# Performance work log

Measured on AMD Instinct MI355X. Metric: run time of the kernel, lower is better.

Reference implementation:

```python
import jax, jax.numpy as jnp
import numpy as np

H = 12      # num attention heads
W = 128     # one-sided window size (band = 2W+1), also the chunk size
G = 32      # number of global tokens (positions 0..G-1)
NEG = -1e9


def setup_inputs() -> dict:
    key = jax.random.key(0)
    ks = jax.random.split(key, 9)
    B, S, D = 1, 4096, 768
    std = 0.02
    f32 = jnp.float32
    return {
        "hidden_states": jax.random.normal(ks[0], (B, S, D), f32),
        "Wq": jax.random.normal(ks[1], (D, D), f32) * std,
        "bq": jnp.zeros((D,), f32),
        "Wk": jax.random.normal(ks[2], (D, D), f32) * std,
        "bk": jnp.zeros((D,), f32),
        "Wv": jax.random.normal(ks[3], (D, D), f32) * std,
        "bv": jnp.zeros((D,), f32),
        "Wo": jax.random.normal(ks[4], (D, D), f32) * std,
        "bo": jnp.zeros((D,), f32),
    }


def _longformer_attn(hidden, Wq, bq, Wk, bk, Wv, bv, Wo, bo):
    B, S, D = hidden.shape
    dh = D // H
    scale = jnp.asarray(dh, hidden.dtype) ** -0.5

    def proj(Wm, bm):
        return (hidden @ Wm + bm).reshape(B, S, H, dh).transpose(0, 2, 1, 3)  # [B,H,S,dh]

    q = proj(Wq, bq) * scale
    k = proj(Wk, bk)
    v = proj(Wv, bv)

    nc = S // W  # number of query chunks
    q_ch = q.reshape(B, H, nc, W, dh)

    # pad keys/values by one chunk on each side; chunk c sees keys [c*W - W, c*W + 2W)
    kp = jnp.pad(k, ((0, 0), (0, 0), (W, W), (0, 0)))
    vp = jnp.pad(v, ((0, 0), (0, 0), (W, W), (0, 0)))
    idx = (jnp.arange(nc) * W)[:, None] + jnp.arange(3 * W)[None, :]  # [nc, 3W] into padded seq
    k_ch = kp[:, :, idx]  # [B,H,nc,3W,dh]
    v_ch = vp[:, :, idx]

    # banded scores via chunked matmul: [B,H,nc,W,3W]
    band = jnp.einsum('bhcqd,bhckd->bhcqk', q_ch, k_ch)

    # exact band mask |i-j| <= W: with local query qi and local key kj (global j = c*W + kj - W)
    qi = jnp.arange(W)[:, None]           # [W,1]
    kj = jnp.arange(3 * W)[None, :]       # [1,3W]
    in_band = (kj >= qi) & (kj <= qi + 2 * W)                     # [W,3W]
    j = (jnp.arange(nc) * W)[:, None, None] + kj[None] - W        # [nc,1,3W] global key index
    valid = in_band[None] & (j >= G) & (j < S)                    # [nc,W,3W]; j<G handled via global path
    band = jnp.where(valid[None, None], band, NEG)
    band = band.reshape(B, H, S, 3 * W)

    # every query also attends to the G global keys
    gsc = jnp.einsum('bhsd,bhgd->bhsg', q, k[:, :, :G])           # [B,H,S,G]
    scores = jnp.concatenate([gsc, band], axis=-1)                # [B,H,S,G+3W]
    probs = jax.nn.softmax(scores, axis=-1)

    out = jnp.einsum('bhsg,bhgd->bhsd', probs[..., :G], v[:, :, :G])
    pb = probs[..., G:].reshape(B, H, nc, W, 3 * W)
    out = out + jnp.einsum('bhcqk,bhckd->bhcqd', pb, v_ch).reshape(B, H, S, dh)

    # global queries attend to everything (full attention on G rows)
    gq_probs = jax.nn.softmax(jnp.einsum('bhgd,bhsd->bhgs', q[:, :, :G], k), axis=-1)
    out_g = jnp.einsum('bhgs,bhsd->bhgd', gq_probs, v)
    out = out.at[:, :, :G].set(out_g)

    out = out.transpose(0, 2, 1, 3).reshape(B, S, D)
    return out @ Wo + bo


def reference(hidden_states, Wq, bq, Wk, bk, Wv, bv, Wo, bo):
    return _longformer_attn(hidden_states, Wq, bq, Wk, bk, Wv, bv, Wo, bo)
```

## Files before the change

### kernel.cpp

```cpp
#include <hip/hip_runtime.h>
#include <stdint.h>

#define S_LEN 4096
#define DMOD  768
#define NH    12
#define DH    64
#define GG    32
#define NEGBIG (-1e9f)

typedef _Float16 f16;
typedef f16 f16x8 __attribute__((ext_vector_type(8)));
typedef f16 f16x4 __attribute__((ext_vector_type(4)));
typedef float f32x4 __attribute__((ext_vector_type(4)));
typedef uint32_t u32;

#define OFF_H16   ((size_t)0)
#define OFF_WT    ((size_t)6291456)
#define OFF_Q     ((size_t)11010048)
#define OFF_K     ((size_t)17301504)
#define OFF_V     ((size_t)23592960)
#define OFF_VT    ((size_t)29884416)
#define OFF_ATT   ((size_t)36175872)
#define OFF_GQO   ((size_t)42467328)
#define OFF_GQL   ((size_t)44040192)

__device__ __forceinline__ void gld_lds16(const void* g, void* l) {
  typedef __attribute__((address_space(3))) u32 lds_u32;
  typedef __attribute__((address_space(1))) u32 glb_u32;
  __builtin_amdgcn_global_load_lds((glb_u32*)(uintptr_t)g,
                                   (lds_u32*)(u32)(uintptr_t)l, 16, 0, 0);
}

__global__ __launch_bounds__(256) void prep_kernel(
    const float* __restrict__ hs,
    const float* __restrict__ Wq, const float* __restrict__ Wk,
    const float* __restrict__ Wv, const float* __restrict__ Wo,
    f16* __restrict__ h16, f16* __restrict__ wt)
{
  const int b = blockIdx.x;
  const int t = threadIdx.x;
  if (b < 576) {
    __shared__ float tile[64][65];
    const int w = b / 144, r2 = b % 144;
    const int n0 = (r2 % 12) * 64, k0 = (r2 / 12) * 64;
    const float* W = (w==0) ? Wq : (w==1) ? Wk : (w==2) ? Wv : Wo;
    f16* WT = wt + (size_t)w * DMOD * DMOD;
    #pragma unroll
    for (int rnd = 0; rnd < 4; ++rnd) {
      const int lin = rnd * 1024 + t * 4;
      const int r = lin >> 6, c = lin & 63;
      const float4 vv = *(const float4*)(W + (size_t)(k0 + r) * DMOD + n0 + c);
      tile[r][c+0] = vv.x; tile[r][c+1] = vv.y; tile[r][c+2] = vv.z; tile[r][c+3] = vv.w;
    }
    __syncthreads();
    #pragma unroll
    for (int rnd = 0; rnd < 2; ++rnd) {
      const int lin = rnd * 256 + t;
      const int n = lin >> 3, kc = (lin & 7) * 8;
      f16x8 o;
      #pragma unroll
      for (int j = 0; j < 8; ++j) o[j] = (f16)tile[kc + j][n];
      *(f16x8*)(WT + (size_t)(n0 + n) * DMOD + k0 + kc) = o;
    }
  } else {
    const size_t idx = (size_t)(b - 576) * 2048 + (size_t)t * 8;
    const float4 a = *(const float4*)(hs + idx);
    const float4 c = *(const float4*)(hs + idx + 4);
    f16x8 o;
    o[0]=(f16)a.x; o[1]=(f16)a.y; o[2]=(f16)a.z; o[3]=(f16)a.w;
    o[4]=(f16)c.x; o[5]=(f16)c.y; o[6]=(f16)c.z; o[7]=(f16)c.w;
    *(f16x8*)(h16 + idx) = o;
  }
}

__global__ __launch_bounds__(256) void gemm_qkv(
    const f16* __restrict__ A, const f16* __restrict__ wt,
    const float* __restrict__ bq, const float* __restrict__ bk, const float* __restrict__ bv,
    f16* __restrict__ q16, f16* __restrict__ k16, f16* __restrict__ v16)
{
  __shared__ __align__(16) f16 At[3][4096];
  __shared__ __align__(16) f16 Bt[3][4096];
  const int z = blockIdx.z;
  const f16* Wt = wt + (size_t)z * DMOD * DMOD;
  const float* bias = (z==0) ? bq : (z==1) ? bk : bv;
  f16* outp = (z==0) ? q16 : (z==1) ? k16 : v16;
  const float scale = (z==0) ? 0.125f : 1.0f;

  const int tid = threadIdx.x;
  const int lane = tid & 63, wid = tid >> 6;
  const int quad = lane >> 4, l15 = lane & 15;
  const int n0 = blockIdx.x * 128, m0 = blockIdx.y * 128;
  const int wm = (wid >> 1) * 64, wn = (wid & 1) * 64;

  f32x4 acc[4][4];
  #pragma unroll
  for (int i=0;i<4;++i)
    #pragma unroll
    for (int j=0;j<4;++j) acc[i][j] = (f32x4){0.f,0.f,0.f,0.f};

  const int lin0 = tid, lin1 = tid + 256;
  const int ar0 = ((lin0>>6)<<4) + (lin0&15), ac0 = ((lin0>>4)&3)*8;
  const int ar1 = ((lin1>>6)<<4) + (lin1&15), ac1 = ((lin1>>4)&3)*8;
  const f16* Ab = A  + (size_t)m0 * DMOD;
  const f16* Bb = Wt + (size_t)n0 * DMOD;

  gld_lds16(Ab + (size_t)ar0*DMOD + ac0, &At[0][lin0*8]);
  gld_lds16(Ab + (size_t)ar1*DMOD + ac1, &At[0][lin1*8]);
  gld_lds16(Bb + (size_t)ar0*DMOD + ac0, &Bt[0][lin0*8]);
  gld_lds16(Bb + (size_t)ar1*DMOD + ac1, &Bt[0][lin1*8]);

  int cur = 0;
  #pragma unroll 3
  for (int k = 0; k < 24; ++k) {
    const int nxt = (cur == 2) ? 0 : cur + 1;
    if (k < 23) {
      const int k0 = (k + 1) * 32;
      gld_lds16(Ab + (size_t)ar0*DMOD + k0 + ac0, &At[nxt][lin0*8]);
      gld_lds16(Ab + (size_t)ar1*DMOD + k0 + ac1, &At[nxt][lin1*8]);
      gld_lds16(Bb + (size_t)ar0*DMOD + k0 + ac0, &Bt[nxt][lin0*8]);
      gld_lds16(Bb + (size_t)ar1*DMOD + k0 + ac1, &Bt[nxt][lin1*8]);
      asm volatile("s_waitcnt vmcnt(4) lgkmcnt(0)" ::: "memory");
    } else {
      asm volatile("s_waitcnt vmcnt(0) lgkmcnt(0)" ::: "memory");
    }
    __builtin_amdgcn_s_barrier();
    f16x8 af[4], bf[4];
    #pragma unroll
    for (int i=0;i<4;++i) {
      af[i] = *(const f16x8*)(&At[cur][((wm>>4)+i)*512 + lane*8]);
      bf[i] = *(const f16x8*)(&Bt[cur][((wn>>4)+i)*512 + lane*8]);
    }
    #pragma unroll
    for (int i=0;i<4;++i)
      #pragma unroll
      for (int j=0;j<4;++j)
        acc[i][j] = __builtin_amdgcn_mfma_f32_16x16x32_f16(af[i], bf[j], acc[i][j], 0, 0, 0);
    cur = nxt;
  }

  #pragma unroll
  for (int j=0;j<4;++j) {
    const int col = n0 + wn + j*16 + l15;
    const float bcol = bias[col];
    const int h = col >> 6, d = col & 63;
    #pragma unroll
    for (int i=0;i<4;++i) {
      const int rbase = m0 + wm + i*16 + quad*4;
      f16* dst = outp + ((size_t)h * S_LEN + rbase) * DH + d;
      #pragma unroll
      for (int r=0;r<4;++r)
        dst[(size_t)r * DH] = (f16)((acc[i][j][r] + bcol) * scale);
    }
  }
}

__global__ __launch_bounds__(256) void gemm_out(
    const f16* __restrict__ A, const f16* __restrict__ Wt,
    const float* __restrict__ bo, float* __restrict__ outp)
{
  __shared__ __align__(16) f16 At[3][4096];
  __shared__ __align__(16) f16 Bt[3][2048];
  const int tid = threadIdx.x;
  const int lane = tid & 63, wid = tid >> 6;
  const int quad = lane >> 4, l15 = lane & 15;
  const int n0 = blockIdx.x * 64, m0 = blockIdx.y * 128;
  const int wm = (wid >> 1) * 64, wn = (wid & 1) * 32;

  f32x4 acc[4][2];
  #pragma unroll
  for (int i=0;i<4;++i)
    #pragma unroll
    for (int j=0;j<2;++j) acc[i][j] = (f32x4){0.f,0.f,0.f,0.f};

  const int lin0 = tid, lin1 = tid + 256;
  const int ar0 = ((lin0>>6)<<4) + (lin0&15), ac0 = ((lin0>>4)&3)*8;
  const int ar1 = ((lin1>>6)<<4) + (lin1&15), ac1 = ((lin1>>4)&3)*8;
  const f16* Ab = A  + (size_t)m0 * DMOD;
  const f16* Bb = Wt + (size_t)n0 * DMOD;

  gld_lds16(Ab + (size_t)ar0*DMOD + ac0, &At[0][lin0*8]);
  gld_lds16(Ab + (size_t)ar1*DMOD + ac1, &At[0][lin1*8]);
  gld_lds16(Bb + (size_t)ar0*DMOD + ac0, &Bt[0][lin0*8]);

  int cur = 0;
  #pragma unroll 3
  for (int k = 0; k < 24; ++k) {
    const int nxt = (cur == 2) ? 0 : cur + 1;
    if (k < 23) {
      const int k0 = (k + 1) * 32;
      gld_lds16(Ab + (size_t)ar0*DMOD + k0 + ac0, &At[nxt][lin0*8]);
      gld_lds16(Ab + (size_t)ar1*DMOD + k0 + ac1, &At[nxt][lin1*8]);
      gld_lds16(Bb + (size_t)ar0*DMOD + k0 + ac0, &Bt[nxt][lin0*8]);
      asm volatile("s_waitcnt vmcnt(3) lgkmcnt(0)" ::: "memory");
    } else {
      asm volatile("s_waitcnt vmcnt(0) lgkmcnt(0)" ::: "memory");
    }
    __builtin_amdgcn_s_barrier();
    f16x8 af[4], bf[2];
    #pragma unroll
    for (int i=0;i<4;++i)
      af[i] = *(const f16x8*)(&At[cur][((wm>>4)+i)*512 + lane*8]);
    #pragma unroll
    for (int j=0;j<2;++j)
      bf[j] = *(const f16x8*)(&Bt[cur][((wn>>4)+j)*512 + lane*8]);
    #pragma unroll
    for (int i=0;i<4;++i)
      #pragma unroll
      for (int j=0;j<2;++j)
        acc[i][j] = __builtin_amdgcn_mfma_f32_16x16x32_f16(af[i], bf[j], acc[i][j], 0, 0, 0);
    cur = nxt;
  }

  #pragma unroll
  for (int j=0;j<2;++j) {
    const int col = n0 + wn + j*16 + l15;
    const float bcol = bo[col];
    #pragma unroll
    for (int i=0;i<4;++i) {
      const int rbase = m0 + wm + i*16 + quad*4;
      #pragma unroll
      for (int r=0;r<4;++r)
        outp[(size_t)(rbase + r) * DMOD + col] = acc[i][j][r] + bcol;
    }
  }
}

__global__ __launch_bounds__(256) void v_transpose(const f16* __restrict__ v16,
                                                   f16* __restrict__ vt16)
{
  __shared__ f16 tile[64][72];
  const int st = blockIdx.x, h = blockIdx.y;
  const int t = threadIdx.x;
  const f16* src = v16 + (size_t)h * S_LEN * DH + (size_t)st * 64 * DH;
  #pragma unroll
  for (int rnd=0; rnd<2; ++rnd) {
    const int lin = rnd*256 + t;
    const int r = lin >> 3, c = (lin & 7) * 8;
    const f16x8 vv = *(const f16x8*)(src + (size_t)r * DH + c);
    #pragma unroll
    for (int j=0;j<8;++j) tile[r][c+j] = vv[j];
  }
  __syncthreads();
  f16* dst = vt16 + (size_t)h * DH * S_LEN + (size_t)st * 64;
  #pragma unroll
  for (int rnd=0; rnd<2; ++rnd) {
    const int lin = rnd*256 + t;
    const int d = lin >> 3, c = (lin & 7) * 8;
    f16x8 vv;
    #pragma unroll
    for (int j=0;j<8;++j) vv[j] = tile[c+j][d];
    *(f16x8*)(dst + (size_t)d * S_LEN + c) = vv;
  }
}

__global__ __launch_bounds__(256) void band_attn(
    const f16* __restrict__ q16, const f16* __restrict__ k16,
    const f16* __restrict__ vt16, f16* __restrict__ att16,
    float* __restrict__ o_part, float* __restrict__ l_part)
{
  __shared__ __align__(16) char smem[27648];
  __shared__ float lbuf[4][32];
  const int h = blockIdx.y;
  const int tid = threadIdx.x, lane = tid & 63, wid = tid >> 6;
  const int quad = lane >> 4, l15 = lane & 15;
  f16* P = (f16*)smem + wid * 1280;

  const f16* qh = q16 + (size_t)h * S_LEN * DH;
  const f16* kh = k16 + (size_t)h * S_LEN * DH;
  const f16* vh = vt16 + (size_t)h * DH * S_LEN;

  const bool is_gq = (blockIdx.x >= 127);
  const int gr0 = is_gq ? 0 : (blockIdx.x + 1) * 32;
  const int sp  = blockIdx.x - 127;

  f16x8 aq[2][2];
  #pragma unroll
  for (int mt=0;mt<2;++mt)
    #pragma unroll
    for (int ks=0;ks<2;++ks)
      aq[mt][ks] = *(const f16x8*)(qh + (size_t)(gr0 + mt*16 + l15)*DH + ks*32 + quad*8);

  f32x4 accO[2][4];
  float lacc[2][4];
  #pragma unroll
  for (int mt=0;mt<2;++mt) {
    #pragma unroll
    for (int n=0;n<4;++n) accO[mt][n] = (f32x4){0.f,0.f,0.f,0.f};
    #pragma unroll
    for (int r=0;r<4;++r) lacc[mt][r] = 0.f;
  }

  const int tstart = is_gq ? wid*2     : (wid==0) ? 0 : (wid==1) ? 2 : (wid==2) ? 5 : 8;
  const int tend   = is_gq ? wid*2 + 2 : (wid==0) ? 2 : (wid==1) ? 5 : (wid==2) ? 8 : 10;

  for (int t = tstart; t < tend; ++t) {
    int j0;
    if (is_gq) {
      j0 = sp*256 + t*32;
    } else if (t > 0) {
      j0 = gr0 - 128 + (t-1)*32;
      if (j0 <= 0 || j0 >= S_LEN) continue;
    } else {
      j0 = 0;
    }
    f16x8 bk[2][2];
    #pragma unroll
    for (int nt=0;nt<2;++nt) {
      const int key = j0 + nt*16 + l15;
      #pragma unroll
      for (int ks=0;ks<2;++ks)
        bk[nt][ks] = *(const f16x8*)(kh + (size_t)key*DH + ks*32 + quad*8);
    }
    f32x4 sc[2][2];
    #pragma unroll
    for (int mt=0;mt<2;++mt)
      #pragma unroll
      for (int nt=0;nt<2;++nt) {
        f32x4 s = __builtin_amdgcn_mfma_f32_16x16x32_f16(aq[mt][0], bk[nt][0],
                                                         (f32x4){0.f,0.f,0.f,0.f}, 0,0,0);
        sc[mt][nt] = __builtin_amdgcn_mfma_f32_16x16x32_f16(aq[mt][1], bk[nt][1], s, 0,0,0);
      }
    if (!is_gq && (t == 1 || t == 9)) {
      #pragma unroll
      for (int nt=0;nt<2;++nt)
        #pragma unroll
        for (int mt=0;mt<2;++mt)
          #pragma unroll
          for (int r=0;r<4;++r) {
            const int e = (nt*16 + l15) - (mt*16 + quad*4 + r);
            const bool ok = (t == 1) ? (e >= 0) : (e <= 0);
            if (!ok) sc[mt][nt][r] = NEGBIG;
          }
    }
    #pragma unroll
    for (int mt=0;mt<2;++mt)
      #pragma unroll
      for (int r=0;r<4;++r) {
        sc[mt][0][r] = __expf(sc[mt][0][r]);
        sc[mt][1][r] = __expf(sc[mt][1][r]);
        lacc[mt][r] += sc[mt][0][r] + sc[mt][1][r];
      }
    #pragma unroll
    for (int mt=0;mt<2;++mt)
      #pragma unroll
      for (int nt=0;nt<2;++nt)
        #pragma unroll
        for (int r=0;r<4;++r)
          P[(mt*16 + quad*4 + r)*40 + nt*16 + l15] = (f16)sc[mt][nt][r];
    asm volatile("s_waitcnt lgkmcnt(0)" ::: "memory");
    f16x8 ap[2];
    #pragma unroll
    for (int mt=0;mt<2;++mt)
      ap[mt] = *(const f16x8*)(P + (mt*16 + l15)*40 + quad*8);
    #pragma unroll
    for (int n=0;n<4;++n) {
      const f16x8 bv = *(const f16x8*)(vh + (size_t)(n*16 + l15)*S_LEN + j0 + quad*8);
      #pragma unroll
      for (int mt=0;mt<2;++mt)
        accO[mt][n] = __builtin_amdgcn_mfma_f32_16x16x32_f16(ap[mt], bv, accO[mt][n], 0,0,0);
    }
  }

  #pragma unroll
  for (int mt=0;mt<2;++mt)
    #pragma unroll
    for (int r=0;r<4;++r) {
      float v = lacc[mt][r];
      v += __shfl_xor(v, 1, 64);
      v += __shfl_xor(v, 2, 64);
      v += __shfl_xor(v, 4, 64);
      v += __shfl_xor(v, 8, 64);
      lacc[mt][r] = v;
    }

  __syncthreads();
  float* mbuf = (float*)smem;
  if (wid > 0) {
    #pragma unroll
    for (int mt=0;mt<2;++mt)
      #pragma unroll
      for (int n=0;n<4;++n)
        *(f32x4*)&mbuf[((wid-1)*64 + n*16 + l15)*36 + mt*16 + quad*4] = accO[mt][n];
  }
  if (l15 == 0) {
    #pragma unroll
    for (int mt=0;mt<2;++mt)
      #pragma unroll
      for (int r=0;r<4;++r)
        lbuf[wid][mt*16 + quad*4 + r] = lacc[mt][r];
  }
  __syncthreads();
  if (wid == 0) {
    #pragma unroll
    for (int w=0;w<3;++w)
      #pragma unroll
      for (int mt=0;mt<2;++mt)
        #pragma unroll
        for (int n=0;n<4;++n)
          accO[mt][n] += *(const f32x4*)&mbuf[(w*64 + n*16 + l15)*36 + mt*16 + quad*4];
    if (is_gq) {
      const int base = (h*16 + sp)*32;
      #pragma unroll
      for (int mt=0;mt<2;++mt)
        #pragma unroll
        for (int r=0;r<4;++r) {
          const int row = mt*16 + quad*4 + r;
          if (l15 == 0)
            l_part[base+row] = lbuf[0][row] + lbuf[1][row] + lbuf[2][row] + lbuf[3][row];
          #pragma unroll
          for (int n=0;n<4;++n)
            o_part[(size_t)(base+row)*DH + n*16 + l15] = accO[mt][n][r];
        }
    } else {
      #pragma unroll
      for (int mt=0;mt<2;++mt)
        #pragma unroll
        for (int r=0;r<4;++r) {
          const int row = mt*16 + quad*4 + r;
          const float lt = lbuf[0][row] + lbuf[1][row] + lbuf[2][row] + lbuf[3][row];
          const float inv = 1.f / lt;
          const int s = gr0 + row;
          #pragma unroll
          for (int n=0;n<4;++n)
            att16[(size_t)s * DMOD + h*DH + n*16 + l15] = (f16)(accO[mt][n][r] * inv);
        }
    }
  }
}

__global__ __launch_bounds__(256) void gq_merge(
    const float* __restrict__ o_part, const float* __restrict__ l_part,
    f16* __restrict__ att16)
{
  const int h = blockIdx.x;
  const int t = threadIdx.x;
  for (int u = t; u < 512; u += 256) {
    const int row = u >> 4, c4 = u & 15;
    float4 s = {0.f,0.f,0.f,0.f};
    float l = 0.f;
    for (int sp=0;sp<16;++sp) {
      const int base = (h*16 + sp)*32 + row;
      const float4 v = *(const float4*)&o_part[(size_t)base*DH + c4*4];
      s.x += v.x; s.y += v.y; s.z += v.z; s.w += v.w;
      l += l_part[base];
    }
    const float inv = 1.f / l;
    f16x4 o;
    o[0] = (f16)(s.x*inv); o[1] = (f16)(s.y*inv);
    o[2] = (f16)(s.z*inv); o[3] = (f16)(s.w*inv);
    *(f16x4*)&att16[(size_t)row * DMOD + h*DH + c4*4] = o;
  }
}

extern "C" void kernel_launch(void* const* d_in, const int* in_sizes, int n_in,
                              void* d_out, int out_size, void* d_ws, size_t ws_size,
                              hipStream_t stream)
{
  const float* hs = (const float*)d_in[0];
  const float* Wq = (const float*)d_in[1];
  const float* bq = (const float*)d_in[2];
  const float* Wk = (const float*)d_in[3];
  const float* bk = (const float*)d_in[4];
  const float* Wv = (const float*)d_in[5];
  const float* bv = (const float*)d_in[6];
  const float* Wo = (const float*)d_in[7];
  const float* bo = (const float*)d_in[8];
  float* out = (float*)d_out;
  char* ws = (char*)d_ws;
  f16* h16  = (f16*)(ws + OFF_H16);
  f16* wt   = (f16*)(ws + OFF_WT);
  f16* q16  = (f16*)(ws + OFF_Q);
  f16* k16  = (f16*)(ws + OFF_K);
  f16* v16  = (f16*)(ws + OFF_V);
  f16* vt16 = (f16*)(ws + OFF_VT);
  f16* att16= (f16*)(ws + OFF_ATT);
  float* gqo = (float*)(ws + OFF_GQO);
  float* gql = (float*)(ws + OFF_GQL);

  prep_kernel<<<2112, 256, 0, stream>>>(hs, Wq, Wk, Wv, Wo, h16, wt);
  gemm_qkv<<<dim3(6,32,3), 256, 0, stream>>>(h16, wt, bq, bk, bv, q16, k16, v16);
  v_transpose<<<dim3(64,12), 256, 0, stream>>>(v16, vt16);
  band_attn<<<dim3(143,12), 256, 0, stream>>>(q16, k16, vt16, att16, gqo, gql);
  gq_merge<<<12, 256, 0, stream>>>(gqo, gql, att16);
  gemm_out<<<dim3(12,32), 256, 0, stream>>>(att16, wt + (size_t)3*DMOD*DMOD, bo, out);
}
```

Baseline: 183.2 us.

## Fuse V transpose into QKV GEMM epilogue and give each wave independent band rows

The V projection epilogue now writes its output directly in transposed [h][d][s] layout, which removes the separate v_transpose kernel and its round trip through memory. band_attn is reorganised so each wave owns its own 32-row query group (or global-query split) for all key tiles, instead of four waves splitting the key tiles of one group. That drops the LDS cross-wave reduction and both barriers, and the grid shrinks from 143 to 36 blocks per head. The risks are strided 8-byte stores in the V epilogue and fewer blocks, which may lower occupancy and latency hiding.

```diff
diff --git a/kernel.cpp b/kernel.cpp
--- a/kernel.cpp
+++ b/kernel.cpp
@@ -18,7 +18,6 @@
 #define OFF_WT    ((size_t)6291456)
 #define OFF_Q     ((size_t)11010048)
 #define OFF_K     ((size_t)17301504)
-#define OFF_V     ((size_t)23592960)
 #define OFF_VT    ((size_t)29884416)
 #define OFF_ATT   ((size_t)36175872)
 #define OFF_GQO   ((size_t)42467328)
@@ -76,14 +75,13 @@
 __global__ __launch_bounds__(256) void gemm_qkv(
     const f16* __restrict__ A, const f16* __restrict__ wt,
     const float* __restrict__ bq, const float* __restrict__ bk, const float* __restrict__ bv,
-    f16* __restrict__ q16, f16* __restrict__ k16, f16* __restrict__ v16)
+    f16* __restrict__ q16, f16* __restrict__ k16, f16* __restrict__ vt16)
 {
   __shared__ __align__(16) f16 At[3][4096];
   __shared__ __align__(16) f16 Bt[3][4096];
   const int z = blockIdx.z;
   const f16* Wt = wt + (size_t)z * DMOD * DMOD;
   const float* bias = (z==0) ? bq : (z==1) ? bk : bv;
-  f16* outp = (z==0) ? q16 : (z==1) ? k16 : v16;
   const float scale = (z==0) ? 0.125f : 1.0f;
 
   const int tid = threadIdx.x;
@@ -138,18 +136,36 @@
     cur = nxt;
   }
 
-  #pragma unroll
-  for (int j=0;j<4;++j) {
-    const int col = n0 + wn + j*16 + l15;
-    const float bcol = bias[col];
-    const int h = col >> 6, d = col & 63;
-    #pragma unroll
-    for (int i=0;i<4;++i) {
-      const int rbase = m0 + wm + i*16 + quad*4;
-      f16* dst = outp + ((size_t)h * S_LEN + rbase) * DH + d;
-      #pragma unroll
-      for (int r=0;r<4;++r)
-        dst[(size_t)r * DH] = (f16)((acc[i][j][r] + bcol) * scale);
+  if (z < 2) {
+    f16* outp = (z==0) ? q16 : k16;
+    #pragma unroll
+    for (int j=0;j<4;++j) {
+      const int col = n0 + wn + j*16 + l15;
+      const float bcol = bias[col];
+      const int h = col >> 6, d = col & 63;
+      #pragma unroll
+      for (int i=0;i<4;++i) {
+        const int rbase = m0 + wm + i*16 + quad*4;
+        f16* dst = outp + ((size_t)h * S_LEN + rbase) * DH + d;
+        #pragma unroll
+        for (int r=0;r<4;++r)
+          dst[(size_t)r * DH] = (f16)((acc[i][j][r] + bcol) * scale);
+      }
+    }
+  } else {
+    #pragma unroll
+    for (int j=0;j<4;++j) {
+      const int col = n0 + wn + j*16 + l15;
+      const float bcol = bias[col];
+      const int h = col >> 6, d = col & 63;
+      #pragma unroll
+      for (int i=0;i<4;++i) {
+        const int rbase = m0 + wm + i*16 + quad*4;
+        f16x4 o;
+        #pragma unroll
+        for (int r=0;r<4;++r) o[r] = (f16)(acc[i][j][r] + bcol);
+        *(f16x4*)(vt16 + ((size_t)h * DH + d) * S_LEN + rbase) = o;
+      }
     }
   }
 }
@@ -225,54 +241,34 @@
   }
 }
 
-__global__ __launch_bounds__(256) void v_transpose(const f16* __restrict__ v16,
-                                                   f16* __restrict__ vt16)
-{
-  __shared__ f16 tile[64][72];
-  const int st = blockIdx.x, h = blockIdx.y;
-  const int t = threadIdx.x;
-  const f16* src = v16 + (size_t)h * S_LEN * DH + (size_t)st * 64 * DH;
-  #pragma unroll
-  for (int rnd=0; rnd<2; ++rnd) {
-    const int lin = rnd*256 + t;
-    const int r = lin >> 3, c = (lin & 7) * 8;
-    const f16x8 vv = *(const f16x8*)(src + (size_t)r * DH + c);
-    #pragma unroll
-    for (int j=0;j<8;++j) tile[r][c+j] = vv[j];
-  }
-  __syncthreads();
-  f16* dst = vt16 + (size_t)h * DH * S_LEN + (size_t)st * 64;
-  #pragma unroll
-  for (int rnd=0; rnd<2; ++rnd) {
-    const int lin = rnd*256 + t;
-    const int d = lin >> 3, c = (lin & 7) * 8;
-    f16x8 vv;
-    #pragma unroll
-    for (int j=0;j<8;++j) vv[j] = tile[c+j][d];
-    *(f16x8*)(dst + (size_t)d * S_LEN + c) = vv;
-  }
-}
-
 __global__ __launch_bounds__(256) void band_attn(
     const f16* __restrict__ q16, const f16* __restrict__ k16,
     const f16* __restrict__ vt16, f16* __restrict__ att16,
     float* __restrict__ o_part, float* __restrict__ l_part)
 {
-  __shared__ __align__(16) char smem[27648];
-  __shared__ float lbuf[4][32];
+  __shared__ __align__(16) f16 Pbuf[4][1280];
   const int h = blockIdx.y;
   const int tid = threadIdx.x, lane = tid & 63, wid = tid >> 6;
   const int quad = lane >> 4, l15 = lane & 15;
-  f16* P = (f16*)smem + wid * 1280;
+  f16* P = &Pbuf[wid][0];
+
+  const int bx = blockIdx.x;
+  const bool is_gq = (bx >= 32);
+  int gr0 = 0, sp = 0, tcount;
+  if (is_gq) {
+    sp = (bx - 32) * 4 + wid;
+    tcount = 8;
+  } else {
+    const int sub = bx * 4 + wid;
+    if (sub == 0) return;
+    gr0 = sub * 32;
+    tcount = 10;
+  }
 
   const f16* qh = q16 + (size_t)h * S_LEN * DH;
   const f16* kh = k16 + (size_t)h * S_LEN * DH;
   const f16* vh = vt16 + (size_t)h * DH * S_LEN;
 
-  const bool is_gq = (blockIdx.x >= 127);
-  const int gr0 = is_gq ? 0 : (blockIdx.x + 1) * 32;
-  const int sp  = blockIdx.x - 127;
-
   f16x8 aq[2][2];
   #pragma unroll
   for (int mt=0;mt<2;++mt)
@@ -290,10 +286,7 @@
     for (int r=0;r<4;++r) lacc[mt][r] = 0.f;
   }
 
-  const int tstart = is_gq ? wid*2     : (wid==0) ? 0 : (wid==1) ? 2 : (wid==2) ? 5 : 8;
-  const int tend   = is_gq ? wid*2 + 2 : (wid==0) ? 2 : (wid==1) ? 5 : (wid==2) ? 8 : 10;
-
-  for (int t = tstart; t < tend; ++t) {
+  for (int t = 0; t < tcount; ++t) {
     int j0;
     if (is_gq) {
       j0 = sp*256 + t*32;
@@ -373,58 +366,29 @@
       lacc[mt][r] = v;
     }
 
-  __syncthreads();
-  float* mbuf = (float*)smem;
-  if (wid > 0) {
-    #pragma unroll
-    for (int mt=0;mt<2;++mt)
-      #pragma unroll
-      for (int n=0;n<4;++n)
-        *(f32x4*)&mbuf[((wid-1)*64 + n*16 + l15)*36 + mt*16 + quad*4] = accO[mt][n];
-  }
-  if (l15 == 0) {
-    #pragma unroll
-    for (int mt=0;mt<2;++mt)
-      #pragma unroll
-      for (int r=0;r<4;++r)
-        lbuf[wid][mt*16 + quad*4 + r] = lacc[mt][r];
-  }
-  __syncthreads();
-  if (wid == 0) {
-    #pragma unroll
-    for (int w=0;w<3;++w)
-      #pragma unroll
-      for (int mt=0;mt<2;++mt)
+  if (is_gq) {
+    const int base = (h*16 + sp)*32;
+    #pragma unroll
+    for (int mt=0;mt<2;++mt)
+      #pragma unroll
+      for (int r=0;r<4;++r) {
+        const int row = mt*16 + quad*4 + r;
+        if (l15 == 0) l_part[base+row] = lacc[mt][r];
         #pragma unroll
         for (int n=0;n<4;++n)
-          accO[mt][n] += *(const f32x4*)&mbuf[(w*64 + n*16 + l15)*36 + mt*16 + quad*4];
-    if (is_gq) {
-      const int base = (h*16 + sp)*32;
-      #pragma unroll
-      for (int mt=0;mt<2;++mt)
-        #pragma unroll
-        for (int r=0;r<4;++r) {
-          const int row = mt*16 + quad*4 + r;
-          if (l15 == 0)
-            l_part[base+row] = lbuf[0][row] + lbuf[1][row] + lbuf[2][row] + lbuf[3][row];
-          #pragma unroll
-          for (int n=0;n<4;++n)
-            o_part[(size_t)(base+row)*DH + n*16 + l15] = accO[mt][n][r];
-        }
-    } else {
-      #pragma unroll
-      for (int mt=0;mt<2;++mt)
-        #pragma unroll
-        for (int r=0;r<4;++r) {
-          const int row = mt*16 + quad*4 + r;
-          const float lt = lbuf[0][row] + lbuf[1][row] + lbuf[2][row] + lbuf[3][row];
-          const float inv = 1.f / lt;
-          const int s = gr0 + row;
-          #pragma unroll
-          for (int n=0;n<4;++n)
-            att16[(size_t)s * DMOD + h*DH + n*16 + l15] = (f16)(accO[mt][n][r] * inv);
-        }
-    }
+          o_part[(size_t)(base+row)*DH + n*16 + l15] = accO[mt][n][r];
+      }
+  } else {
+    #pragma unroll
+    for (int mt=0;mt<2;++mt)
+      #pragma unroll
+      for (int r=0;r<4;++r) {
+        const float inv = 1.f / lacc[mt][r];
+        const int s = gr0 + mt*16 + quad*4 + r;
+        #pragma unroll
+        for (int n=0;n<4;++n)
+          att16[(size_t)s * DMOD + h*DH + n*16 + l15] = (f16)(accO[mt][n][r] * inv);
+      }
   }
 }
 
@@ -471,16 +435,14 @@
   f16* wt   = (f16*)(ws + OFF_WT);
   f16* q16  = (f16*)(ws + OFF_Q);
   f16* k16  = (f16*)(ws + OFF_K);
-  f16* v16  = (f16*)(ws + OFF_V);
   f16* vt16 = (f16*)(ws + OFF_VT);
   f16* att16= (f16*)(ws + OFF_ATT);
   float* gqo = (float*)(ws + OFF_GQO);
   float* gql = (float*)(ws + OFF_GQL);
 
   prep_kernel<<<2112, 256, 0, stream>>>(hs, Wq, Wk, Wv, Wo, h16, wt);
-  gemm_qkv<<<dim3(6,32,3), 256, 0, stream>>>(h16, wt, bq, bk, bv, q16, k16, v16);
-  v_transpose<<<dim3(64,12), 256, 0, stream>>>(v16, vt16);
-  band_attn<<<dim3(143,12), 256, 0, stream>>>(q16, k16, vt16, att16, gqo, gql);
+  gemm_qkv<<<dim3(6,32,3), 256, 0, stream>>>(h16, wt, bq, bk, bv, q16, k16, vt16);
+  band_attn<<<dim3(36,12), 256, 0, stream>>>(q16, k16, vt16, att16, gqo, gql);
   gq_merge<<<12, 256, 0, stream>>>(gqo, gql, att16);
   gemm_out<<<dim3(12,32), 256, 0, stream>>>(att16, wt + (size_t)3*DMOD*DMOD, bo, out);
 }
```

Result: faster. 170.7 us (-6.8%).
